# Optimization experiments

Hardware: AMD Instinct MI355X
Metric: run time of the kernel (lower is better)

## Reference

```python
import jax, jax.numpy as jnp
import numpy as np

N_HEADS = 16
N_KV_HEADS = 4
HEAD_DIM = 128  # d_model // n_heads = 2048 // 16
ROPE_THETA = 10000.0


def _rope_cos_sin(T, D, dtype):
    inv_freq = 1.0 / (ROPE_THETA ** (jnp.arange(0, D, 2, dtype=jnp.float32) / D))
    t = jnp.arange(T, dtype=jnp.float32)
    freqs = jnp.outer(t, inv_freq)               # [T, D/2]
    emb = jnp.concatenate([freqs, freqs], axis=-1)  # [T, D]
    return jnp.cos(emb).astype(dtype), jnp.sin(emb).astype(dtype)


def _rotate_half(x):
    x1, x2 = jnp.split(x, 2, axis=-1)
    return jnp.concatenate([-x2, x1], axis=-1)


def setup_inputs() -> dict:
    key = jax.random.key(0)
    k1, k2, k3, k4, k5 = jax.random.split(key, 5)
    B, T, C = 2, 2048, 2048
    H, KV, D = N_HEADS, N_KV_HEADS, HEAD_DIM
    s = 0.02
    return {
        "x": jax.random.normal(k1, (B, T, C), dtype=jnp.float32),
        "Wq": jax.random.normal(k2, (C, H * D), dtype=jnp.float32) * s,
        "Wk": jax.random.normal(k3, (C, KV * D), dtype=jnp.float32) * s,
        "Wv": jax.random.normal(k4, (C, KV * D), dtype=jnp.float32) * s,
        "Wo": jax.random.normal(k5, (H * D, C), dtype=jnp.float32) * s,
    }


def reference(x, Wq, Wk, Wv, Wo):
    B, T, C = x.shape
    H, KV, D = N_HEADS, N_KV_HEADS, HEAD_DIM
    G = H // KV
    scale = D ** -0.5

    q = (x @ Wq).reshape(B, T, H, D).transpose(0, 2, 1, 3)    # [B,H,T,D]
    k = (x @ Wk).reshape(B, T, KV, D).transpose(0, 2, 1, 3)   # [B,KV,T,D]
    v = (x @ Wv).reshape(B, T, KV, D).transpose(0, 2, 1, 3)   # [B,KV,T,D]

    cos, sin = _rope_cos_sin(T, D, x.dtype)  # [T,D] each, broadcasts over B,H
    q = q * cos + _rotate_half(q) * sin
    k = k * cos + _rotate_half(k) * sin

    # repeat_interleave kv heads to match query heads
    k = jnp.repeat(k, G, axis=1)  # [B,H,T,D]
    v = jnp.repeat(v, G, axis=1)  # [B,H,T,D]

    scores = jnp.einsum('bhqd,bhkd->bhqk', q, k) * scale  # [B,H,T,T]
    causal = jnp.tril(jnp.ones((T, T), dtype=bool))
    scores = jnp.where(causal, scores, jnp.finfo(scores.dtype).min)
    attn = jax.nn.softmax(scores, axis=-1)

    out = jnp.einsum('bhqk,bhkd->bhqd', attn, v)           # [B,H,T,D]
    out = out.transpose(0, 2, 1, 3).reshape(B, T, H * D)    # [B,T,C]
    return out @ Wo
```

## Files before the change

kernel.cpp:

```cpp
#include <hip/hip_runtime.h>
#include <cstdint>
#include <cstddef>

typedef __attribute__((ext_vector_type(4))) float f32x4;
typedef __attribute__((ext_vector_type(8))) short s16x8;
typedef __attribute__((ext_vector_type(4))) short s16x4;

#define B_  2
#define T_  2048
#define C_  2048
#define H_  16
#define KV_ 4
#define D_  128
#define M_  4096

static __device__ __forceinline__ float bf2f(ushort u){
  union { float f; uint32_t u; } x; x.u = ((uint32_t)u) << 16; return x.f;
}
static __device__ __forceinline__ ushort f2bf(float f){
  union { float f; uint32_t u; } x; x.f = f;
  uint32_t r = x.u + 0x7FFF + ((x.u >> 16) & 1);
  return (ushort)(r >> 16);
}

static __device__ __forceinline__ void gl_lds16(const ushort* g, ushort* s){
  __builtin_amdgcn_global_load_lds((const __attribute__((address_space(1))) void*)g,
                                   (__attribute__((address_space(3))) void*)s, 16, 0, 0);
}

__global__ void cvt_f32_bf16(const float* __restrict__ in, ushort* __restrict__ out, int n4){
  int idx = blockIdx.x * blockDim.x + threadIdx.x;
  int stride = gridDim.x * blockDim.x;
  for (int i = idx; i < n4; i += stride){
    float4 v = ((const float4*)in)[i];
    s16x4 o;
    o[0] = (short)f2bf(v.x); o[1] = (short)f2bf(v.y);
    o[2] = (short)f2bf(v.z); o[3] = (short)f2bf(v.w);
    ((s16x4*)out)[i] = o;
  }
}

__global__ void transpose_cvt(const float* __restrict__ W, ushort* __restrict__ Wt, int K, int N){
  __shared__ float tile[32][33];
  int n0 = blockIdx.x * 32, k0 = blockIdx.y * 32;
  int tx = threadIdx.x, ty = threadIdx.y;
  #pragma unroll
  for (int r = 0; r < 4; r++)
    tile[ty + 8*r][tx] = W[(size_t)(k0 + ty + 8*r) * N + n0 + tx];
  __syncthreads();
  #pragma unroll
  for (int r = 0; r < 4; r++)
    Wt[(size_t)(n0 + ty + 8*r) * K + k0 + tx] = f2bf(tile[tx][ty + 8*r]);
}

template<int MODE>
__global__ __launch_bounds__(512)
void gemm_deep(const ushort* __restrict__ A, const ushort* __restrict__ Bt,
               void* __restrict__ C0, void* __restrict__ C1, void* __restrict__ C2,
               int N, int Kd, int nbx){
  __shared__ __align__(16) ushort Abuf[4][8192];
  __shared__ __align__(16) ushort Bbuf[4][8192];
  int tid = threadIdx.x, w = tid >> 6, l = tid & 63;
  int l15 = l & 15, l4 = l >> 4;

  int cpx = gridDim.x >> 3;
  int logical = (blockIdx.x & 7) * cpx + (blockIdx.x >> 3);
  int bx = logical % nbx, by = logical / nbx;
  int rblk = by * 128, cblk = bx * 128;
  int wm = w & 1, wn = w >> 1;

  int sr = tid >> 3;
  int sc = ((tid & 7) * 8) ^ ((sr & 7) << 3);
  const ushort* gA = A  + (size_t)(rblk + sr) * Kd + sc;
  const ushort* gB = Bt + (size_t)(cblk + sr) * Kd + sc;
  size_t rowK = (size_t)64 * Kd;
  int wb = w * 512;

  auto stage = [&](int t){
    int bsel = t & 3; int koff = t * 64;
    gl_lds16(gA + koff,        &Abuf[bsel][wb]);
    gl_lds16(gA + rowK + koff, &Abuf[bsel][4096 + wb]);
    gl_lds16(gB + koff,        &Bbuf[bsel][wb]);
    gl_lds16(gB + rowK + koff, &Bbuf[bsel][4096 + wb]);
  };

  int arow = wm * 64 + l15;
  int brow = wn * 32 + l15;
  int kx0 = (l4 * 8) ^ ((l15 & 7) << 3);
  int kx1 = (32 + l4 * 8) ^ ((l15 & 7) << 3);

  f32x4 acc[4][2] = {};

  auto phase = [&](int t, int dostage, int vm){
    const ushort* Ab = Abuf[t & 3];
    const ushort* Bb = Bbuf[t & 3];
    s16x8 a[4][2], b[2][2];
    #pragma unroll
    for (int m = 0; m < 4; m++){
      a[m][0] = *(const s16x8*)(Ab + (arow + m*16) * 64 + kx0);
      a[m][1] = *(const s16x8*)(Ab + (arow + m*16) * 64 + kx1);
    }
    #pragma unroll
    for (int n = 0; n < 2; n++){
      b[n][0] = *(const s16x8*)(Bb + (brow + n*16) * 64 + kx0);
      b[n][1] = *(const s16x8*)(Bb + (brow + n*16) * 64 + kx1);
    }
    if (dostage) stage(t + 3);
    if (vm == 8)      { asm volatile("s_waitcnt vmcnt(8)" ::: "memory"); }
    else if (vm == 4) { asm volatile("s_waitcnt vmcnt(4)" ::: "memory"); }
    else if (vm == 0) { asm volatile("s_waitcnt vmcnt(0)" ::: "memory"); }
    if (vm >= 0) __builtin_amdgcn_sched_barrier(0);
    __builtin_amdgcn_s_barrier();
    asm volatile("s_waitcnt lgkmcnt(0)" ::: "memory");
    __builtin_amdgcn_sched_barrier(0);
    __builtin_amdgcn_s_setprio(1);
    #pragma unroll
    for (int m = 0; m < 4; m++)
      #pragma unroll
      for (int n = 0; n < 2; n++){
        acc[m][n] = __builtin_amdgcn_mfma_f32_16x16x32_bf16(a[m][0], b[n][0], acc[m][n], 0, 0, 0);
        acc[m][n] = __builtin_amdgcn_mfma_f32_16x16x32_bf16(a[m][1], b[n][1], acc[m][n], 0, 0, 0);
      }
    __builtin_amdgcn_s_setprio(0);
    __builtin_amdgcn_s_barrier();
  };

  stage(0); stage(1); stage(2);
  asm volatile("s_waitcnt vmcnt(8)" ::: "memory");
  __builtin_amdgcn_s_barrier();

  int nt = Kd >> 6;
  for (int t = 0; t < nt - 3; ++t) phase(t, 1, 8);
  phase(nt - 3, 0, 4);
  phase(nt - 2, 0, 0);
  phase(nt - 1, 0, -1);

  #pragma unroll
  for (int m = 0; m < 4; m++){
    #pragma unroll
    for (int n = 0; n < 2; n++){
      #pragma unroll
      for (int j = 0; j < 4; j++){
        int row = rblk + wm*64 + m*16 + l4*4 + j;
        int col = cblk + wn*32 + n*16 + l15;
        float v = acc[m][n][j];
        if (MODE == 0){
          ((float*)C0)[(size_t)row * N + col] = v;
        } else {
          int t = row & (T_ - 1), bb = row >> 11;
          ushort bv = f2bf(v);
          if (cblk < 2048){
            int hh = col >> 7, d = col & 127;
            ((ushort*)C0)[(((size_t)(bb * H_ + hh)) * T_ + t) * D_ + d] = bv;
          } else if (cblk < 2560){
            int c2 = col - 2048;
            int hh = c2 >> 7, d = c2 & 127;
            ((ushort*)C1)[(((size_t)(bb * KV_ + hh)) * T_ + t) * D_ + d] = bv;
          } else {
            int c2 = col - 2560;
            int hh = c2 >> 7, d = c2 & 127;
            ((ushort*)C2)[(((size_t)(bb * KV_ + hh)) * D_ + d) * T_ + t] = bv;
          }
        }
      }
    }
  }
}

__global__ __launch_bounds__(256)
void rope_inplace2(ushort* __restrict__ X, float scale){
  int tr = threadIdx.x >> 4;
  int j  = threadIdx.x & 15;
  int t  = blockIdx.x * 16 + tr;
  int bh = blockIdx.y;
  ushort* row = X + ((size_t)bh * T_ + t) * D_;
  s16x4 lo = *(const s16x4*)(row + j*4);
  s16x4 hi = *(const s16x4*)(row + 64 + j*4);
  s16x4 olo, ohi;
  #pragma unroll
  for (int i = 0; i < 4; i++){
    int d = j*4 + i;
    float invf = exp2f(-(float)d * 0.2076205059304602f);
    float s, c;
    __sincosf((float)t * invf, &s, &c);
    float q1 = bf2f((ushort)lo[i]);
    float q2 = bf2f((ushort)hi[i]);
    olo[i] = (short)f2bf((q1 * c - q2 * s) * scale);
    ohi[i] = (short)f2bf((q2 * c + q1 * s) * scale);
  }
  *(s16x4*)(row + j*4) = olo;
  *(s16x4*)(row + 64 + j*4) = ohi;
}

__global__ __launch_bounds__(512, 4)
void attn_kernel4(const ushort* __restrict__ Q, const ushort* __restrict__ Kc,
                  const ushort* __restrict__ Vt, ushort* __restrict__ O){
  __shared__ __align__(16) ushort Ks[64 * 128];
  __shared__ __align__(16) ushort Vs[128 * 64];
  __shared__ __align__(16) ushort Ps[8 * 16 * 64];
  int bid = blockIdx.x;
  int i  = bid >> 3;
  int qt = (i < 32) ? (63 - i) : (i - 32);
  int sub = bid & 7;
  int b = sub >> 2, kvh = sub & 3;
  int tid = threadIdx.x, w = tid >> 6, l = tid & 63;
  int l15 = l & 15, l4 = l >> 4;
  int sw3 = (l15 & 7) << 3;
  int q0 = qt * 32;
  int hq = kvh * 4 + (w >> 1);
  int qrow0 = q0 + (w & 1) * 16;
  int qrow = qrow0 + l15;

  s16x8 qf[4];
  const ushort* qbase = Q + (((size_t)(b * H_ + hq)) * T_ + qrow) * D_;
  #pragma unroll
  for (int kk = 0; kk < 4; kk++)
    qf[kk] = *(const s16x8*)(qbase + kk * 32 + l4 * 8);

  f32x4 oacc[8] = {};
  float mrun = -1e30f;
  float rsum = 0.f;
  const float THR = 11.5415603f;
  ushort* Pw = Ps + w * (16 * 64) + l15 * 64;

  const ushort* kbase = Kc + ((size_t)(b * KV_ + kvh)) * T_ * D_;
  const ushort* vbase = Vt + ((size_t)(b * KV_ + kvh)) * D_ * T_;
  int jmax = (q0 + 31) >> 6;

  int kr0 = tid >> 4, kcb = tid & 15;
  int vd0 = tid >> 3, vtb = tid & 7;
  int ksoff = kr0 * 128 + ((kcb * 8) ^ ((kr0 & 7) << 3));
  int vsoff = vd0 * 64  + ((vtb * 8) ^ ((vd0 & 7) << 3));
  const ushort* kg = kbase + (size_t)kr0 * D_ + kcb * 8;
  const ushort* vg = vbase + (size_t)vd0 * T_ + vtb * 8;

  s16x8 kreg0, kreg1, vreg0, vreg1;
  kreg0 = *(const s16x8*)(kg);
  kreg1 = *(const s16x8*)(kg + (size_t)32 * D_);
  vreg0 = *(const s16x8*)(vg);
  vreg1 = *(const s16x8*)(vg + (size_t)64 * T_);

  for (int jt = 0; jt <= jmax; jt++){
    __syncthreads();
    *(s16x8*)(Ks + ksoff)            = kreg0;
    *(s16x8*)(Ks + ksoff + 32 * 128) = kreg1;
    *(s16x8*)(Vs + vsoff)            = vreg0;
    *(s16x8*)(Vs + vsoff + 64 * 64)  = vreg1;
    __syncthreads();
    if (jt < jmax){
      int k1 = (jt + 1) * 64;
      kreg0 = *(const s16x8*)(kg + (size_t)k1 * D_);
      kreg1 = *(const s16x8*)(kg + (size_t)(k1 + 32) * D_);
      vreg0 = *(const s16x8*)(vg + k1);
      vreg1 = *(const s16x8*)(vg + (size_t)64 * T_ + k1);
    }
    int k0 = jt * 64;

    f32x4 sacc[4] = {};
    __builtin_amdgcn_s_setprio(1);
    #pragma unroll
    for (int kk = 0; kk < 4; kk++){
      #pragma unroll
      for (int n = 0; n < 4; n++){
        s16x8 kf = *(const s16x8*)(Ks + (16*n + l15) * 128 + ((kk*32 + l4*8) ^ sw3));
        sacc[n] = __builtin_amdgcn_mfma_f32_16x16x32_bf16(kf, qf[kk], sacc[n], 0, 0, 0);
      }
    }
    __builtin_amdgcn_s_setprio(0);
    if (jt == jmax){
      #pragma unroll
      for (int n = 0; n < 4; n++)
        #pragma unroll
        for (int j = 0; j < 4; j++){
          int kcol = k0 + 16*n + 4*l4 + j;
          if (kcol > qrow) sacc[n][j] = -1e30f;
        }
    }
    float mloc = -1e30f;
    #pragma unroll
    for (int n = 0; n < 4; n++)
      #pragma unroll
      for (int j = 0; j < 4; j++)
        mloc = fmaxf(mloc, sacc[n][j]);
    if (__any((int)(mloc > mrun + THR))){
      float m2 = fmaxf(mloc, __shfl_xor(mloc, 16));
      m2 = fmaxf(m2, __shfl_xor(m2, 32));
      float mnew = fmaxf(mrun, m2);
      float alpha = exp2f(mrun - mnew);
      mrun = mnew;
      rsum *= alpha;
      #pragma unroll
      for (int n8 = 0; n8 < 8; n8++)
        #pragma unroll
        for (int j = 0; j < 4; j++)
          oacc[n8][j] *= alpha;
    }
    #pragma unroll
    for (int n = 0; n < 4; n++){
      s16x4 pk;
      #pragma unroll
      for (int j = 0; j < 4; j++){
        float p = exp2f(sacc[n][j] - mrun);
        rsum += p;
        pk[j] = (short)f2bf(p);
      }
      *(s16x4*)(Pw + ((16*n + 4*l4) ^ sw3)) = pk;
    }
    __builtin_amdgcn_s_setprio(1);
    #pragma unroll
    for (int kk = 0; kk < 2; kk++){
      s16x8 pf = *(const s16x8*)(Pw + ((kk*32 + l4*8) ^ sw3));
      #pragma unroll
      for (int n8 = 0; n8 < 8; n8++){
        s16x8 vf = *(const s16x8*)(Vs + (16*n8 + l15) * 64 + ((kk*32 + l4*8) ^ sw3));
        oacc[n8] = __builtin_amdgcn_mfma_f32_16x16x32_bf16(vf, pf, oacc[n8], 0, 0, 0);
      }
    }
    __builtin_amdgcn_s_setprio(0);
  }

  rsum += __shfl_xor(rsum, 16);
  rsum += __shfl_xor(rsum, 32);
  float inv = 1.f / rsum;
  ushort* obase = O + ((size_t)(b * T_ + qrow)) * C_ + hq * D_ + 4*l4;
  #pragma unroll
  for (int n8 = 0; n8 < 8; n8++){
    s16x4 ov;
    #pragma unroll
    for (int j = 0; j < 4; j++)
      ov[j] = (short)f2bf(oacc[n8][j] * inv);
    *(s16x4*)(obase + 16*n8) = ov;
  }
}

extern "C" void kernel_launch(void* const* d_in, const int* in_sizes, int n_in,
                              void* d_out, int out_size, void* d_ws, size_t ws_size,
                              hipStream_t stream){
  const float* x  = (const float*)d_in[0];
  const float* Wq = (const float*)d_in[1];
  const float* Wk = (const float*)d_in[2];
  const float* Wv = (const float*)d_in[3];
  const float* Wo = (const float*)d_in[4];
  float* out = (float*)d_out;

  char* ws = (char*)d_ws;
  size_t off = 0;
  auto alloc = [&](size_t bytes)->void*{
    void* p = ws + off; off += (bytes + 255) & ~(size_t)255; return p;
  };
  ushort* xb   = (ushort*)alloc((size_t)M_ * C_ * 2);
  ushort* Wcat = (ushort*)alloc((size_t)3072 * 2048 * 2);
  ushort* Wot  = (ushort*)alloc((size_t)2048 * 2048 * 2);
  ushort* Qb   = (ushort*)alloc((size_t)B_ * H_ * T_ * D_ * 2);
  ushort* Kb   = (ushort*)alloc((size_t)B_ * KV_ * T_ * D_ * 2);
  ushort* Vtb  = (ushort*)alloc((size_t)B_ * KV_ * T_ * D_ * 2);
  ushort* Ob   = (ushort*)alloc((size_t)M_ * C_ * 2);

  cvt_f32_bf16<<<2048, 256, 0, stream>>>(x, xb, M_ * C_ / 4);
  transpose_cvt<<<dim3(64, 64), dim3(32, 8), 0, stream>>>(Wq, Wcat, 2048, 2048);
  transpose_cvt<<<dim3(16, 64), dim3(32, 8), 0, stream>>>(Wk, Wcat + (size_t)2048*2048, 2048, 512);
  transpose_cvt<<<dim3(16, 64), dim3(32, 8), 0, stream>>>(Wv, Wcat + (size_t)2560*2048, 2048, 512);
  transpose_cvt<<<dim3(64, 64), dim3(32, 8), 0, stream>>>(Wo, Wot, 2048, 2048);

  gemm_deep<1><<<768, 512, 0, stream>>>(xb, Wcat, Qb, Kb, Vtb, 3072, 2048, 24);

  rope_inplace2<<<dim3(T_/16, B_ * H_),  256, 0, stream>>>(Qb, 0.08838834764831845f * 1.4426950408889634f);
  rope_inplace2<<<dim3(T_/16, B_ * KV_), 256, 0, stream>>>(Kb, 1.0f);

  attn_kernel4<<<512, 512, 0, stream>>>(Qb, Kb, Vtb, Ob);

  gemm_deep<0><<<512, 512, 0, stream>>>(Ob, Wot, out, nullptr, nullptr, 2048, 2048, 16);
}
```

Baseline: 223.0 us.

## Use larger 256-row GEMM tiles with double buffering and one-wave grid

Replaces the 128x128 four-stage-pipelined GEMM with a templated kernel that uses 256xBN tiles (BN=192 for QKV, 128 for the output projection) and two-stage double buffering. Each grid is now 256 blocks, one per CU, with a new block-to-tile swizzle. The aim is more reuse per loaded byte and no tail wave. The cost is a shallower prefetch (full vmcnt(0) wait each iteration), more registers per thread, and less latency hiding. The QKV epilogue now routes on the column rather than the block start, because a 192-wide tile can straddle the Q/K/V boundaries.

```diff
diff --git a/kernel.cpp b/kernel.cpp
--- a/kernel.cpp
+++ b/kernel.cpp
@@ -53,106 +53,104 @@
     Wt[(size_t)(n0 + ty + 8*r) * K + k0 + tx] = f2bf(tile[tx][ty + 8*r]);
 }
 
-template<int MODE>
+template<int MODE, int BN>
 __global__ __launch_bounds__(512)
-void gemm_deep(const ushort* __restrict__ A, const ushort* __restrict__ Bt,
-               void* __restrict__ C0, void* __restrict__ C1, void* __restrict__ C2,
-               int N, int Kd, int nbx){
-  __shared__ __align__(16) ushort Abuf[4][8192];
-  __shared__ __align__(16) ushort Bbuf[4][8192];
+void gemm_v2(const ushort* __restrict__ A, const ushort* __restrict__ Bt,
+             void* __restrict__ C0, void* __restrict__ C1, void* __restrict__ C2,
+             int N, int Kd){
+  constexpr int NF = BN / 32;
+  constexpr int BV = BN / 64;
+  __shared__ __align__(16) ushort Abuf[2][16384];
+  __shared__ __align__(16) ushort Bbuf[2][BN * 64];
   int tid = threadIdx.x, w = tid >> 6, l = tid & 63;
   int l15 = l & 15, l4 = l >> 4;
 
-  int cpx = gridDim.x >> 3;
-  int logical = (blockIdx.x & 7) * cpx + (blockIdx.x >> 3);
-  int bx = logical % nbx, by = logical / nbx;
-  int rblk = by * 128, cblk = bx * 128;
-  int wm = w & 1, wn = w >> 1;
+  int x = blockIdx.x & 7, i = blockIdx.x >> 3;
+  int by = (x & 3) * 4 + (i & 3);
+  int bx = (x >> 2) * 8 + (i >> 2);
+  int rblk = by * 256, cblk = bx * BN;
+  int wm = w >> 1, wn = w & 1;
 
   int sr = tid >> 3;
   int sc = ((tid & 7) * 8) ^ ((sr & 7) << 3);
   const ushort* gA = A  + (size_t)(rblk + sr) * Kd + sc;
   const ushort* gB = Bt + (size_t)(cblk + sr) * Kd + sc;
-  size_t rowK = (size_t)64 * Kd;
   int wb = w * 512;
 
   auto stage = [&](int t){
-    int bsel = t & 3; int koff = t * 64;
-    gl_lds16(gA + koff,        &Abuf[bsel][wb]);
-    gl_lds16(gA + rowK + koff, &Abuf[bsel][4096 + wb]);
-    gl_lds16(gB + koff,        &Bbuf[bsel][wb]);
-    gl_lds16(gB + rowK + koff, &Bbuf[bsel][4096 + wb]);
+    int cur = t & 1; int koff = t * 64;
+    #pragma unroll
+    for (int v = 0; v < 4; v++)
+      gl_lds16(gA + (size_t)v * 64 * Kd + koff, &Abuf[cur][v * 4096 + wb]);
+    #pragma unroll
+    for (int v = 0; v < BV; v++)
+      gl_lds16(gB + (size_t)v * 64 * Kd + koff, &Bbuf[cur][v * 4096 + wb]);
   };
 
   int arow = wm * 64 + l15;
-  int brow = wn * 32 + l15;
-  int kx0 = (l4 * 8) ^ ((l15 & 7) << 3);
-  int kx1 = (32 + l4 * 8) ^ ((l15 & 7) << 3);
-
-  f32x4 acc[4][2] = {};
-
-  auto phase = [&](int t, int dostage, int vm){
-    const ushort* Ab = Abuf[t & 3];
-    const ushort* Bb = Bbuf[t & 3];
-    s16x8 a[4][2], b[2][2];
+  int brow = wn * (BN / 2) + l15;
+  int sw = (l15 & 7) << 3;
+  int kx0 = (l4 * 8) ^ sw;
+  int kx1 = (32 + l4 * 8) ^ sw;
+
+  f32x4 acc[4][NF] = {};
+
+  stage(0);
+  asm volatile("s_waitcnt vmcnt(0)" ::: "memory");
+  __builtin_amdgcn_s_barrier();
+
+  int nt = Kd >> 6;
+  for (int t = 0; t < nt; ++t){
+    if (t + 1 < nt) stage(t + 1);
+    const ushort* Ab = Abuf[t & 1];
+    const ushort* Bb = Bbuf[t & 1];
+    s16x8 a[4][2], b[NF][2];
     #pragma unroll
     for (int m = 0; m < 4; m++){
       a[m][0] = *(const s16x8*)(Ab + (arow + m*16) * 64 + kx0);
       a[m][1] = *(const s16x8*)(Ab + (arow + m*16) * 64 + kx1);
     }
     #pragma unroll
-    for (int n = 0; n < 2; n++){
+    for (int n = 0; n < NF; n++){
       b[n][0] = *(const s16x8*)(Bb + (brow + n*16) * 64 + kx0);
       b[n][1] = *(const s16x8*)(Bb + (brow + n*16) * 64 + kx1);
     }
-    if (dostage) stage(t + 3);
-    if (vm == 8)      { asm volatile("s_waitcnt vmcnt(8)" ::: "memory"); }
-    else if (vm == 4) { asm volatile("s_waitcnt vmcnt(4)" ::: "memory"); }
-    else if (vm == 0) { asm volatile("s_waitcnt vmcnt(0)" ::: "memory"); }
-    if (vm >= 0) __builtin_amdgcn_sched_barrier(0);
-    __builtin_amdgcn_s_barrier();
     asm volatile("s_waitcnt lgkmcnt(0)" ::: "memory");
     __builtin_amdgcn_sched_barrier(0);
     __builtin_amdgcn_s_setprio(1);
     #pragma unroll
     for (int m = 0; m < 4; m++)
       #pragma unroll
-      for (int n = 0; n < 2; n++){
+      for (int n = 0; n < NF; n++){
         acc[m][n] = __builtin_amdgcn_mfma_f32_16x16x32_bf16(a[m][0], b[n][0], acc[m][n], 0, 0, 0);
         acc[m][n] = __builtin_amdgcn_mfma_f32_16x16x32_bf16(a[m][1], b[n][1], acc[m][n], 0, 0, 0);
       }
     __builtin_amdgcn_s_setprio(0);
-    __builtin_amdgcn_s_barrier();
-  };
-
-  stage(0); stage(1); stage(2);
-  asm volatile("s_waitcnt vmcnt(8)" ::: "memory");
-  __builtin_amdgcn_s_barrier();
-
-  int nt = Kd >> 6;
-  for (int t = 0; t < nt - 3; ++t) phase(t, 1, 8);
-  phase(nt - 3, 0, 4);
-  phase(nt - 2, 0, 0);
-  phase(nt - 1, 0, -1);
+    if (t + 1 < nt){
+      asm volatile("s_waitcnt vmcnt(0)" ::: "memory");
+      __builtin_amdgcn_sched_barrier(0);
+      __builtin_amdgcn_s_barrier();
+    }
+  }
 
   #pragma unroll
   for (int m = 0; m < 4; m++){
     #pragma unroll
-    for (int n = 0; n < 2; n++){
+    for (int n = 0; n < NF; n++){
       #pragma unroll
       for (int j = 0; j < 4; j++){
         int row = rblk + wm*64 + m*16 + l4*4 + j;
-        int col = cblk + wn*32 + n*16 + l15;
+        int col = cblk + wn*(BN/2) + n*16 + l15;
         float v = acc[m][n][j];
         if (MODE == 0){
           ((float*)C0)[(size_t)row * N + col] = v;
         } else {
           int t = row & (T_ - 1), bb = row >> 11;
           ushort bv = f2bf(v);
-          if (cblk < 2048){
+          if (col < 2048){
             int hh = col >> 7, d = col & 127;
             ((ushort*)C0)[(((size_t)(bb * H_ + hh)) * T_ + t) * D_ + d] = bv;
-          } else if (cblk < 2560){
+          } else if (col < 2560){
             int c2 = col - 2048;
             int hh = c2 >> 7, d = c2 & 127;
             ((ushort*)C1)[(((size_t)(bb * KV_ + hh)) * T_ + t) * D_ + d] = bv;
@@ -362,12 +360,12 @@
   transpose_cvt<<<dim3(16, 64), dim3(32, 8), 0, stream>>>(Wv, Wcat + (size_t)2560*2048, 2048, 512);
   transpose_cvt<<<dim3(64, 64), dim3(32, 8), 0, stream>>>(Wo, Wot, 2048, 2048);
 
-  gemm_deep<1><<<768, 512, 0, stream>>>(xb, Wcat, Qb, Kb, Vtb, 3072, 2048, 24);
+  gemm_v2<1, 192><<<256, 512, 0, stream>>>(xb, Wcat, Qb, Kb, Vtb, 3072, 2048);
 
   rope_inplace2<<<dim3(T_/16, B_ * H_),  256, 0, stream>>>(Qb, 0.08838834764831845f * 1.4426950408889634f);
   rope_inplace2<<<dim3(T_/16, B_ * KV_), 256, 0, stream>>>(Kb, 1.0f);
 
   attn_kernel4<<<512, 512, 0, stream>>>(Qb, Kb, Vtb, Ob);
 
-  gemm_deep<0><<<512, 512, 0, stream>>>(Ob, Wot, out, nullptr, nullptr, 2048, 2048, 16);
-}
+  gemm_v2<0, 128><<<256, 512, 0, stream>>>(Ob, Wot, out, nullptr, nullptr, 2048, 2048);
+}
```

Result: no change. 223.3 us (+0.1%).

## Replace GEMM with 256x256-tile eight-phase ping-pong pipelined kernel

Applied to the files above, without the earlier changes.

Swaps the 128x128-tile GEMM for a 256x256-tile kernel in which each wave computes a 128x64 sub-tile. Loads are split into half-tiles and staged across eight MFMA phases per 128-wide K step, interleaving LDS reads, global-to-LDS copies and barriers. This raises operand reuse per byte loaded and reduces global traffic. The cost is far fewer blocks (192 and 128), which may leave CUs idle, plus more barriers and higher register pressure.

```diff
diff --git a/kernel.cpp b/kernel.cpp
--- a/kernel.cpp
+++ b/kernel.cpp
@@ -53,106 +53,120 @@
     Wt[(size_t)(n0 + ty + 8*r) * K + k0 + tx] = f2bf(tile[tx][ty + 8*r]);
 }
 
+
+#define BAR __builtin_amdgcn_s_barrier()
+#define LGKM0 do{ asm volatile("s_waitcnt lgkmcnt(0)" ::: "memory"); __builtin_amdgcn_sched_barrier(0); }while(0)
+#define VM4 do{ asm volatile("s_waitcnt vmcnt(4)" ::: "memory"); __builtin_amdgcn_sched_barrier(0); }while(0)
+#define VM0 do{ asm volatile("s_waitcnt vmcnt(0)" ::: "memory"); __builtin_amdgcn_sched_barrier(0); }while(0)
+
+#define STG_A(s,h,t) do{ \
+  gl_lds16(gA + (size_t)((h)*128     )*Kd + (t)*64, &Ab[(s)*2+(h)][wb]); \
+  gl_lds16(gA + (size_t)((h)*128 + 64)*Kd + (t)*64, &Ab[(s)*2+(h)][4096+wb]); }while(0)
+#define STG_B(s,h,t) do{ \
+  gl_lds16(gB + (size_t)((h)*128     )*Kd + (t)*64, &Bb[(s)*2+(h)][wb]); \
+  gl_lds16(gB + (size_t)((h)*128 + 64)*Kd + (t)*64, &Bb[(s)*2+(h)][4096+wb]); }while(0)
+
+#define RD_A(P, mh) { const ushort* _pa = (P) + (mh)*4096; \
+  _Pragma("unroll") for (int m_ = 0; m_ < 4; m_++){ \
+    aR[m_][0] = *(const s16x8*)(_pa + (m_*16 + l15)*64 + kx0); \
+    aR[m_][1] = *(const s16x8*)(_pa + (m_*16 + l15)*64 + kx1); } }
+
+#define RD_B(P, nh) { const ushort* _pb = (P) + (brow + (nh)*32)*64; \
+  _Pragma("unroll") for (int n_ = 0; n_ < 2; n_++){ \
+    bR[(nh)*2+n_][0] = *(const s16x8*)(_pb + (n_*16 + l15)*64 + kx0); \
+    bR[(nh)*2+n_][1] = *(const s16x8*)(_pb + (n_*16 + l15)*64 + kx1); } }
+
+#define MQ(mh, nh) { \
+  __builtin_amdgcn_s_setprio(1); \
+  _Pragma("unroll") for (int m_ = 0; m_ < 4; m_++) \
+    _Pragma("unroll") for (int n_ = 0; n_ < 2; n_++){ \
+      acc[(mh)*4+m_][(nh)*2+n_] = __builtin_amdgcn_mfma_f32_16x16x32_bf16(aR[m_][0], bR[(nh)*2+n_][0], acc[(mh)*4+m_][(nh)*2+n_],0,0,0); \
+      acc[(mh)*4+m_][(nh)*2+n_] = __builtin_amdgcn_mfma_f32_16x16x32_bf16(aR[m_][1], bR[(nh)*2+n_][1], acc[(mh)*4+m_][(nh)*2+n_],0,0,0); } \
+  __builtin_amdgcn_s_setprio(0); }
+
 template<int MODE>
-__global__ __launch_bounds__(512)
-void gemm_deep(const ushort* __restrict__ A, const ushort* __restrict__ Bt,
-               void* __restrict__ C0, void* __restrict__ C1, void* __restrict__ C2,
-               int N, int Kd, int nbx){
-  __shared__ __align__(16) ushort Abuf[4][8192];
-  __shared__ __align__(16) ushort Bbuf[4][8192];
+__global__ __launch_bounds__(512, 2)
+void gemm8p(const ushort* __restrict__ A, const ushort* __restrict__ Bt,
+            void* __restrict__ C0, void* __restrict__ C1, void* __restrict__ C2,
+            int N, int Kd, int nbx){
+  __shared__ __align__(16) ushort Ab[4][8192];
+  __shared__ __align__(16) ushort Bb[4][8192];
   int tid = threadIdx.x, w = tid >> 6, l = tid & 63;
   int l15 = l & 15, l4 = l >> 4;
 
   int cpx = gridDim.x >> 3;
   int logical = (blockIdx.x & 7) * cpx + (blockIdx.x >> 3);
   int bx = logical % nbx, by = logical / nbx;
-  int rblk = by * 128, cblk = bx * 128;
-  int wm = w & 1, wn = w >> 1;
+  int rblk = by * 256, cblk = bx * 256;
+  int wm = w >> 2, wn = w & 3;
 
   int sr = tid >> 3;
   int sc = ((tid & 7) * 8) ^ ((sr & 7) << 3);
   const ushort* gA = A  + (size_t)(rblk + sr) * Kd + sc;
   const ushort* gB = Bt + (size_t)(cblk + sr) * Kd + sc;
-  size_t rowK = (size_t)64 * Kd;
   int wb = w * 512;
 
-  auto stage = [&](int t){
-    int bsel = t & 3; int koff = t * 64;
-    gl_lds16(gA + koff,        &Abuf[bsel][wb]);
-    gl_lds16(gA + rowK + koff, &Abuf[bsel][4096 + wb]);
-    gl_lds16(gB + koff,        &Bbuf[bsel][wb]);
-    gl_lds16(gB + rowK + koff, &Bbuf[bsel][4096 + wb]);
-  };
-
-  int arow = wm * 64 + l15;
-  int brow = wn * 32 + l15;
+  const ushort* Ar0 = Ab[wm];
+  const ushort* Ar1 = Ab[2 + wm];
+  const ushort* Br0 = Bb[wn >> 1];
+  const ushort* Br1 = Bb[2 + (wn >> 1)];
+  int brow = (wn & 1) * 64;
   int kx0 = (l4 * 8) ^ ((l15 & 7) << 3);
   int kx1 = (32 + l4 * 8) ^ ((l15 & 7) << 3);
 
-  f32x4 acc[4][2] = {};
-
-  auto phase = [&](int t, int dostage, int vm){
-    const ushort* Ab = Abuf[t & 3];
-    const ushort* Bb = Bbuf[t & 3];
-    s16x8 a[4][2], b[2][2];
-    #pragma unroll
-    for (int m = 0; m < 4; m++){
-      a[m][0] = *(const s16x8*)(Ab + (arow + m*16) * 64 + kx0);
-      a[m][1] = *(const s16x8*)(Ab + (arow + m*16) * 64 + kx1);
-    }
-    #pragma unroll
-    for (int n = 0; n < 2; n++){
-      b[n][0] = *(const s16x8*)(Bb + (brow + n*16) * 64 + kx0);
-      b[n][1] = *(const s16x8*)(Bb + (brow + n*16) * 64 + kx1);
-    }
-    if (dostage) stage(t + 3);
-    if (vm == 8)      { asm volatile("s_waitcnt vmcnt(8)" ::: "memory"); }
-    else if (vm == 4) { asm volatile("s_waitcnt vmcnt(4)" ::: "memory"); }
-    else if (vm == 0) { asm volatile("s_waitcnt vmcnt(0)" ::: "memory"); }
-    if (vm >= 0) __builtin_amdgcn_sched_barrier(0);
-    __builtin_amdgcn_s_barrier();
-    asm volatile("s_waitcnt lgkmcnt(0)" ::: "memory");
-    __builtin_amdgcn_sched_barrier(0);
-    __builtin_amdgcn_s_setprio(1);
-    #pragma unroll
-    for (int m = 0; m < 4; m++)
-      #pragma unroll
-      for (int n = 0; n < 2; n++){
-        acc[m][n] = __builtin_amdgcn_mfma_f32_16x16x32_bf16(a[m][0], b[n][0], acc[m][n], 0, 0, 0);
-        acc[m][n] = __builtin_amdgcn_mfma_f32_16x16x32_bf16(a[m][1], b[n][1], acc[m][n], 0, 0, 0);
-      }
-    __builtin_amdgcn_s_setprio(0);
-    __builtin_amdgcn_s_barrier();
-  };
-
-  stage(0); stage(1); stage(2);
-  asm volatile("s_waitcnt vmcnt(8)" ::: "memory");
-  __builtin_amdgcn_s_barrier();
-
-  int nt = Kd >> 6;
-  for (int t = 0; t < nt - 3; ++t) phase(t, 1, 8);
-  phase(nt - 3, 0, 4);
-  phase(nt - 2, 0, 0);
-  phase(nt - 1, 0, -1);
-
-  #pragma unroll
-  for (int m = 0; m < 4; m++){
-    #pragma unroll
-    for (int n = 0; n < 2; n++){
+  f32x4 acc[8][4] = {};
+  s16x8 aR[4][2], bR[4][2];
+
+  STG_A(0,0,0); STG_A(0,1,0); STG_B(0,0,0); STG_B(0,1,0); STG_B(1,0,1); STG_B(1,1,1);
+  asm volatile("s_waitcnt vmcnt(0)" ::: "memory");
+  BAR;
+
+  int nIter = Kd >> 7;
+  #pragma unroll 1
+  for (int it = 0; it < nIter; ++it){
+    int tv = 2*it + 1, tu2 = 2*it + 2, tv2 = 2*it + 3;
+    bool more = (it + 1 < nIter);
+    RD_A(Ar0, 0); RD_B(Br0, 0);
+    STG_A(1,0,tv); STG_A(1,1,tv);
+    BAR; LGKM0; MQ(0,0); BAR;
+    RD_B(Br0, 1);
+    BAR; LGKM0; MQ(0,1); BAR;
+    RD_A(Ar0, 1);
+    if (more) STG_B(0,0,tu2);
+    BAR; LGKM0; MQ(1,0); BAR;
+    if (more){ STG_B(0,1,tu2); VM4; } else { VM0; }
+    BAR; LGKM0; MQ(1,1); BAR;
+    RD_A(Ar1, 0); RD_B(Br1, 0);
+    if (more) STG_A(0,0,tu2);
+    BAR; LGKM0; MQ(0,0); BAR;
+    RD_B(Br1, 1);
+    if (more) STG_A(0,1,tu2);
+    BAR; LGKM0; MQ(0,1); BAR;
+    RD_A(Ar1, 1);
+    if (more) STG_B(1,0,tv2);
+    BAR; LGKM0; MQ(1,0); BAR;
+    if (more){ STG_B(1,1,tv2); VM4; }
+    BAR; LGKM0; MQ(1,1); BAR;
+  }
+
+  #pragma unroll
+  for (int m = 0; m < 8; m++){
+    #pragma unroll
+    for (int n = 0; n < 4; n++){
       #pragma unroll
       for (int j = 0; j < 4; j++){
-        int row = rblk + wm*64 + m*16 + l4*4 + j;
-        int col = cblk + wn*32 + n*16 + l15;
+        int row = rblk + wm*128 + m*16 + l4*4 + j;
+        int col = cblk + wn*64 + n*16 + l15;
         float v = acc[m][n][j];
         if (MODE == 0){
           ((float*)C0)[(size_t)row * N + col] = v;
         } else {
           int t = row & (T_ - 1), bb = row >> 11;
           ushort bv = f2bf(v);
-          if (cblk < 2048){
+          if (col < 2048){
             int hh = col >> 7, d = col & 127;
             ((ushort*)C0)[(((size_t)(bb * H_ + hh)) * T_ + t) * D_ + d] = bv;
-          } else if (cblk < 2560){
+          } else if (col < 2560){
             int c2 = col - 2048;
             int hh = c2 >> 7, d = c2 & 127;
             ((ushort*)C1)[(((size_t)(bb * KV_ + hh)) * T_ + t) * D_ + d] = bv;
@@ -362,12 +376,12 @@
   transpose_cvt<<<dim3(16, 64), dim3(32, 8), 0, stream>>>(Wv, Wcat + (size_t)2560*2048, 2048, 512);
   transpose_cvt<<<dim3(64, 64), dim3(32, 8), 0, stream>>>(Wo, Wot, 2048, 2048);
 
-  gemm_deep<1><<<768, 512, 0, stream>>>(xb, Wcat, Qb, Kb, Vtb, 3072, 2048, 24);
+  gemm8p<1><<<192, 512, 0, stream>>>(xb, Wcat, Qb, Kb, Vtb, 3072, 2048, 12);
 
   rope_inplace2<<<dim3(T_/16, B_ * H_),  256, 0, stream>>>(Qb, 0.08838834764831845f * 1.4426950408889634f);
   rope_inplace2<<<dim3(T_/16, B_ * KV_), 256, 0, stream>>>(Kb, 1.0f);
 
   attn_kernel4<<<512, 512, 0, stream>>>(Qb, Kb, Vtb, Ob);
 
-  gemm_deep<0><<<512, 512, 0, stream>>>(Ob, Wot, out, nullptr, nullptr, 2048, 2048, 16);
-}
+  gemm8p<0><<<128, 512, 0, stream>>>(Ob, Wot, out, nullptr, nullptr, 2048, 2048, 8);
+}
```

Result: slower. 248.6 us (+11.5%).
